# Kernel tuning notes

Hardware: AMD Instinct MI355X
Metric: run time of the kernel (lower is better)

## Reference

```python
import jax, jax.numpy as jnp
import numpy as np

HID = 128      # hidden_dim
CDIM = 128     # c_dim
NBLK = 5       # n_blocks
RESO = 32      # grid_resolution
G = RESO ** 3  # number of voxels
B, T = 2, 100000


def setup_inputs() -> dict:
    key = jax.random.key(0)
    ks = jax.random.split(key, 8)
    return {
        "points": jax.random.normal(ks[0], (B, T, 3), jnp.float32),
        "index": jax.random.randint(ks[1], (B, 1, T), 0, G, dtype=jnp.int64),
        # fc_pos: Linear(3, 2*HID)
        "fc_pos_w": jax.random.normal(ks[2], (3, 2 * HID), jnp.float32) * 0.1,
        "fc_pos_b": jnp.zeros((2 * HID,), jnp.float32),
        # ResnetBlockFC(2*HID, HID) x NBLK: fc_0 (2H->H), fc_1 (H->H), shortcut (2H->H, no bias)
        "fc0_w": jax.random.normal(ks[3], (NBLK, 2 * HID, HID), jnp.float32) * 0.05,
        "fc0_b": jnp.zeros((NBLK, HID), jnp.float32),
        "fc1_w": jax.random.normal(ks[4], (NBLK, HID, HID), jnp.float32) * 0.05,
        "fc1_b": jnp.zeros((NBLK, HID), jnp.float32),
        "sc_w": jax.random.normal(ks[5], (NBLK, 2 * HID, HID), jnp.float32) * 0.05,
        # fc_c: Linear(HID, CDIM)
        "fc_c_w": jax.random.normal(ks[6], (HID, CDIM), jnp.float32) * 0.05,
        "fc_c_b": jnp.zeros((CDIM,), jnp.float32),
    }


def _resnet_block(x, w0, b0, w1, b1, ws):
    # ResnetBlockFC: net = fc_0(relu(x)); dx = fc_1(relu(net)); out = shortcut(x) + dx
    net = jnp.maximum(x, 0.0) @ w0 + b0
    dx = jnp.maximum(net, 0.0) @ w1 + b1
    return x @ ws + dx


def reference(points, index, fc_pos_w, fc_pos_b, fc0_w, fc0_b, fc1_w, fc1_b, sc_w, fc_c_w, fc_c_b):
    idx = index[:, 0, :]  # [B, T]

    def pool_local(net):
        # scatter_max over voxels, then gather back per point
        seg = jax.vmap(lambda c_b, i_b: jax.ops.segment_max(c_b, i_b, num_segments=G))(net, idx)  # [B,G,H]
        return jnp.take_along_axis(seg, idx[:, :, None], axis=1)  # [B,T,H]; every gathered voxel is non-empty

    net = points @ fc_pos_w + fc_pos_b          # [B,T,2H]
    net = _resnet_block(net, fc0_w[0], fc0_b[0], fc1_w[0], fc1_b[0], sc_w[0])  # [B,T,H]
    for i in range(1, NBLK):
        pooled = pool_local(net)
        net = jnp.concatenate([net, pooled], axis=2)  # [B,T,2H]
        net = _resnet_block(net, fc0_w[i], fc0_b[i], fc1_w[i], fc1_b[i], sc_w[i])

    c = net @ fc_c_w + fc_c_b  # [B,T,CDIM]

    # generate_grid_features: scatter_mean into the 32^3 grid (zeros for empty voxels)
    sums = jax.vmap(lambda c_b, i_b: jax.ops.segment_sum(c_b, i_b, num_segments=G))(c, idx)  # [B,G,CDIM]
    cnts = jax.vmap(lambda i_b: jax.ops.segment_sum(jnp.ones((T,), c.dtype), i_b, num_segments=G))(idx)  # [B,G]
    cnts = cnts[:, :, None]
    mean = jnp.where(cnts > 0, sums / jnp.maximum(cnts, 1.0), 0.0)
    fea_grid = jnp.transpose(mean, (0, 2, 1)).reshape(B, CDIM, RESO, RESO, RESO)
    return fea_grid
```

## Files before the change

kernel.cpp:

```cpp
#include <hip/hip_runtime.h>

#define T_PTS 100000
#define NB 2
#define GCELLS 32768
#define NCELL (NB * GCELLS)
#define HID 128
#define MBLK 64
#define RBPB 1563
#define GRID_RB (NB * RBPB)

typedef __attribute__((ext_vector_type(8))) short bf16x8;
typedef __attribute__((ext_vector_type(4))) float f32x4;

#define MFMA16 __builtin_amdgcn_mfma_f32_16x16x32_bf16

__device__ __forceinline__ unsigned short bf16rne(float f) {
  unsigned u = __float_as_uint(f);
  return (unsigned short)((u + 0x7FFFu + ((u >> 16) & 1u)) >> 16);
}
__device__ __forceinline__ void bf16split(float f, unsigned short& h,
                                          unsigned short& l) {
  h = bf16rne(f);
  l = bf16rne(f - __uint_as_float(((unsigned)h) << 16));
}
__device__ __forceinline__ unsigned packhl(float f) {
  unsigned short h, l;
  bf16split(f, h, l);
  return (((unsigned)h) << 16) | (unsigned)l;
}

union U8 { bf16x8 v; unsigned u[4]; };

__device__ __forceinline__ void up2(unsigned w0, unsigned w1, unsigned& h,
                                    unsigned& l) {
  h = __builtin_amdgcn_perm(w1, w0, 0x07060302u);
  l = __builtin_amdgcn_perm(w1, w0, 0x05040100u);
}

__device__ __forceinline__ void relu2(unsigned qh, unsigned ql, unsigned& rh,
                                      unsigned& rl) {
  const unsigned keep = ((~qh >> 15) & 0x00010001u) * 0xFFFFu;
  rh = qh & keep;
  rl = ql & keep;
}

__device__ __forceinline__ void dma16(const unsigned* g, unsigned* l) {
  __builtin_amdgcn_global_load_lds(
      (const __attribute__((address_space(1))) unsigned*)g,
      (__attribute__((address_space(3))) unsigned*)l, 16, 0, 0);
}

template <int MODE>
__global__ __launch_bounds__(256, 4) void resblock_mfma(
    const void* __restrict__ srcv, const float* __restrict__ posw,
    const float* __restrict__ posb, const unsigned* __restrict__ cell,
    const int* __restrict__ idx, const unsigned short* __restrict__ w0p,
    const float* __restrict__ b0, const unsigned short* __restrict__ w1p,
    const float* __restrict__ b1, const unsigned short* __restrict__ swp,
    unsigned* __restrict__ net_out) {
  __shared__ unsigned lds32[8192];
  const int tid = threadIdx.x;
  const int lane = tid & 63;
  const int wid = tid >> 6;
  const int wc = wid;
  const int b = blockIdx.x / RBPB;
  const int t0 = (blockIdx.x % RBPB) * MBLK;
  const int valid = (T_PTS - t0 < MBLK) ? (T_PTS - t0) : MBLK;

  const int srow = wid * 16 + (lane & 15);
  const int skc4 = (lane >> 4) * 4;
  const int ptc = (t0 + srow < T_PTS) ? srow : (T_PTS - 1 - t0);
  const unsigned* nrowL = nullptr;
  const unsigned* crowL = nullptr;
  float pp0 = 0.f, pp1 = 0.f, pp2 = 0.f;
  if (MODE == 1) {
    const long prow = (long)b * T_PTS + t0 + ptc;
    nrowL = (const unsigned*)srcv + prow * HID;
    crowL = cell + ((long)b * GCELLS + idx[prow]) * HID;
  } else {
    const float* ppp = (const float*)srcv + ((long)b * T_PTS + t0 + ptc) * 3;
    pp0 = ppp[0]; pp1 = ppp[1]; pp2 = ppp[2];
  }

  auto stage_dma = [&](int ks) {
    unsigned* base = &lds32[((ks & 1) << 12) + wid * 256];
    const unsigned* rowp = (ks < 4) ? nrowL : crowL;
    const int ko = ((ks & 3) << 4) + skc4;
    dma16(rowp + ko, base);
    dma16(rowp + 64 + ko, base + 1024);
  };
  auto derive = [&](int ks) {
    const int db = ((ks & 1) << 12) + wid * 256 + lane * 4;
    uint4 qh = *(const uint4*)&lds32[db];
    uint4 ql = *(const uint4*)&lds32[db + 1024];
    uint4 rh, rl;
    relu2(qh.x, ql.x, rh.x, rl.x);
    relu2(qh.y, ql.y, rh.y, rl.y);
    relu2(qh.z, ql.z, rh.z, rl.z);
    relu2(qh.w, ql.w, rh.w, rl.w);
    *(uint4*)&lds32[db + 2048] = rh;
    *(uint4*)&lds32[db + 3072] = rl;
  };
  auto stage0 = [&](int ks) {
    const int kb = ks * 32 + (lane >> 4) * 8;
    float xv[8];
#pragma unroll
    for (int i = 0; i < 8; i += 4) {
      float4 wa = *(const float4*)(posw + kb + i);
      float4 wb = *(const float4*)(posw + 256 + kb + i);
      float4 wcc = *(const float4*)(posw + 512 + kb + i);
      float4 bb = *(const float4*)(posb + kb + i);
      xv[i + 0] = fmaf(pp0, wa.x, fmaf(pp1, wb.x, fmaf(pp2, wcc.x, bb.x)));
      xv[i + 1] = fmaf(pp0, wa.y, fmaf(pp1, wb.y, fmaf(pp2, wcc.y, bb.y)));
      xv[i + 2] = fmaf(pp0, wa.z, fmaf(pp1, wb.z, fmaf(pp2, wcc.z, bb.z)));
      xv[i + 3] = fmaf(pp0, wa.w, fmaf(pp1, wb.w, fmaf(pp2, wcc.w, bb.w)));
    }
    unsigned ph[8];
#pragma unroll
    for (int i = 0; i < 8; ++i) ph[i] = packhl(xv[i]);
    uint4 xh4, xl4, rh4, rl4;
    up2(ph[0], ph[1], xh4.x, xl4.x);
    up2(ph[2], ph[3], xh4.y, xl4.y);
    up2(ph[4], ph[5], xh4.z, xl4.z);
    up2(ph[6], ph[7], xh4.w, xl4.w);
    relu2(xh4.x, xl4.x, rh4.x, rl4.x);
    relu2(xh4.y, xl4.y, rh4.y, rl4.y);
    relu2(xh4.z, xl4.z, rh4.z, rl4.z);
    relu2(xh4.w, xl4.w, rh4.w, rl4.w);
    const int db = ((ks & 1) << 12) + wid * 256 + lane * 4;
    *(uint4*)&lds32[db] = xh4;
    *(uint4*)&lds32[db + 1024] = xl4;
    *(uint4*)&lds32[db + 2048] = rh4;
    *(uint4*)&lds32[db + 3072] = rl4;
  };
  auto load_B = [&](const unsigned short* base, int loOff, int ks, bf16x8* h,
                    bf16x8* l) {
#pragma unroll
    for (int nt = 0; nt < 2; ++nt) {
      const int fi = (ks * 8 + wc * 2 + nt) * 512 + lane * 8;
      h[nt] = *(const bf16x8*)(base + fi);
      l[nt] = *(const bf16x8*)(base + loOff + fi);
    }
  };

  f32x4 accy[4][2], acco[4][2];
#pragma unroll
  for (int i = 0; i < 4; ++i)
#pragma unroll
    for (int j = 0; j < 2; ++j) {
      f32x4 z = {0.f, 0.f, 0.f, 0.f};
      accy[i][j] = z;
      acco[i][j] = z;
    }

  if (MODE == 1) {
    stage_dma(0);
    asm volatile("s_waitcnt vmcnt(0)" ::: "memory");
    derive(0);
  } else {
    stage0(0);
  }
  __syncthreads();

#pragma unroll 1
  for (int ks = 0; ks < 8; ++ks) {
    const int sb = (ks & 1) << 12;
    bf16x8 bh[2], bl[2];
    load_B(w0p, 32768, ks, bh, bl);
    __builtin_amdgcn_s_setprio(1);
#pragma unroll
    for (int mt = 0; mt < 4; ++mt) {
      const unsigned* pr = &lds32[sb + 2048 + mt * 256 + lane * 4];
      bf16x8 rh = *(const bf16x8*)pr;
      bf16x8 rl = *(const bf16x8*)(pr + 1024);
#pragma unroll
      for (int nt = 0; nt < 2; ++nt) {
        accy[mt][nt] = MFMA16(rh, bh[nt], accy[mt][nt], 0, 0, 0);
        accy[mt][nt] = MFMA16(rh, bl[nt], accy[mt][nt], 0, 0, 0);
        accy[mt][nt] = MFMA16(rl, bh[nt], accy[mt][nt], 0, 0, 0);
      }
    }
    __builtin_amdgcn_s_setprio(0);
    load_B(swp, 32768, ks, bh, bl);
    if (MODE == 1 && ks < 7) stage_dma(ks + 1);
    __builtin_amdgcn_s_setprio(1);
#pragma unroll
    for (int mt = 0; mt < 4; ++mt) {
      const unsigned* px = &lds32[sb + mt * 256 + lane * 4];
      bf16x8 xh = *(const bf16x8*)px;
      bf16x8 xl = *(const bf16x8*)(px + 1024);
#pragma unroll
      for (int nt = 0; nt < 2; ++nt) {
        acco[mt][nt] = MFMA16(xh, bh[nt], acco[mt][nt], 0, 0, 0);
        acco[mt][nt] = MFMA16(xh, bl[nt], acco[mt][nt], 0, 0, 0);
        acco[mt][nt] = MFMA16(xl, bh[nt], acco[mt][nt], 0, 0, 0);
      }
    }
    __builtin_amdgcn_s_setprio(0);
    if (ks < 7) {
      if (MODE == 1) {
        asm volatile("s_waitcnt vmcnt(0)" ::: "memory");
        derive(ks + 1);
      } else {
        stage0(ks + 1);
      }
    }
    __syncthreads();
  }

  {
    float b0v[2];
#pragma unroll
    for (int nt = 0; nt < 2; ++nt)
      b0v[nt] = b0[wc * 32 + nt * 16 + (lane & 15)];
#pragma unroll
    for (int mt = 0; mt < 4; ++mt) {
#pragma unroll
      for (int nt = 0; nt < 2; ++nt) {
        const int c = wc * 32 + nt * 16 + (lane & 15);
        const int k2 = c >> 5;
        const int j = c & 7;
        const int lahi = ((c & 31) >> 3) * 16;
#pragma unroll
        for (int r = 0; r < 4; ++r) {
          float h = fmaxf(accy[mt][nt][r] + b0v[nt], 0.f);
          int la = lahi + (lane >> 4) * 4 + r;
          la ^= (la >> 3) & 7;
          lds32[((k2 * 4 + mt) * 64 + la) * 8 + j] = packhl(h);
        }
      }
    }
  }
  __syncthreads();

  {
    const int lar2 = lane ^ ((lane >> 3) & 7);
#pragma unroll
    for (int k2 = 0; k2 < 4; ++k2) {
      bf16x8 ch[2], cl[2];
      load_B(w1p, 16384, k2, ch, cl);
      __builtin_amdgcn_s_setprio(1);
#pragma unroll
      for (int mt = 0; mt < 4; ++mt) {
        const unsigned* p = &lds32[((k2 * 4 + mt) * 64 + lar2) * 8];
        uint4 q1 = *(const uint4*)p;
        uint4 q2 = *(const uint4*)(p + 4);
        unsigned q[8] = {q1.x, q1.y, q1.z, q1.w, q2.x, q2.y, q2.z, q2.w};
        U8 ah, al;
#pragma unroll
        for (int p2 = 0; p2 < 4; ++p2)
          up2(q[2 * p2], q[2 * p2 + 1], ah.u[p2], al.u[p2]);
#pragma unroll
        for (int nt = 0; nt < 2; ++nt) {
          acco[mt][nt] = MFMA16(ah.v, ch[nt], acco[mt][nt], 0, 0, 0);
          acco[mt][nt] = MFMA16(ah.v, cl[nt], acco[mt][nt], 0, 0, 0);
          acco[mt][nt] = MFMA16(al.v, ch[nt], acco[mt][nt], 0, 0, 0);
        }
      }
      __builtin_amdgcn_s_setprio(0);
    }
  }

  {
    float b1v[2];
#pragma unroll
    for (int nt = 0; nt < 2; ++nt)
      b1v[nt] = b1[wc * 32 + nt * 16 + (lane & 15)];
#pragma unroll
    for (int mt = 0; mt < 4; ++mt) {
#pragma unroll
      for (int r = 0; r < 4; ++r) {
        const int row = mt * 16 + (lane >> 4) * 4 + r;
        if (row < valid) {
          unsigned short* op =
              (unsigned short*)(net_out + ((long)b * T_PTS + t0 + row) * HID);
          unsigned short h, l;
          bf16split(acco[mt][0][r] + b1v[0], h, l);
          op[wc * 32 + (lane & 15)] = h;
          op[128 + wc * 32 + (lane & 15)] = l;
          bf16split(acco[mt][1][r] + b1v[1], h, l);
          op[wc * 32 + 16 + (lane & 15)] = h;
          op[128 + wc * 32 + 16 + (lane & 15)] = l;
        }
      }
    }
  }
}

__global__ __launch_bounds__(256, 4) void final_mfma(
    unsigned* __restrict__ net, const unsigned short* __restrict__ wcp,
    const float* __restrict__ bc) {
  __shared__ unsigned lds32[4096];
  const int tid = threadIdx.x;
  const int lane = tid & 63;
  const int wid = tid >> 6;
  const int wc = wid;
  const int b = blockIdx.x / RBPB;
  const int t0 = (blockIdx.x % RBPB) * MBLK;
  const int valid = (T_PTS - t0 < MBLK) ? (T_PTS - t0) : MBLK;

  const int srow = wid * 16 + (lane & 15);
  const int skc4 = (lane >> 4) * 4;
  const int ptc = (t0 + srow < T_PTS) ? srow : (T_PTS - 1 - t0);
  const unsigned* nrowL = net + ((long)b * T_PTS + t0 + ptc) * HID;

  auto stage = [&](int ks) {
    unsigned* base = &lds32[((ks & 1) << 11) + wid * 256];
    const int ko = (ks << 4) + skc4;
    dma16(nrowL + ko, base);
    dma16(nrowL + 64 + ko, base + 1024);
  };
  auto load_B = [&](int ks, bf16x8* h, bf16x8* l) {
#pragma unroll
    for (int nt = 0; nt < 2; ++nt) {
      const int fi = (ks * 8 + wc * 2 + nt) * 512 + lane * 8;
      h[nt] = *(const bf16x8*)(wcp + fi);
      l[nt] = *(const bf16x8*)(wcp + 16384 + fi);
    }
  };

  f32x4 acc[4][2];
#pragma unroll
  for (int i = 0; i < 4; ++i)
#pragma unroll
    for (int j = 0; j < 2; ++j) {
      f32x4 z = {0.f, 0.f, 0.f, 0.f};
      acc[i][j] = z;
    }

  stage(0);
  __syncthreads();

#pragma unroll 1
  for (int ks = 0; ks < 4; ++ks) {
    const int sb = (ks & 1) << 11;
    bf16x8 ch[2], cl[2];
    load_B(ks, ch, cl);
    if (ks < 3) stage(ks + 1);
    __builtin_amdgcn_s_setprio(1);
#pragma unroll
    for (int mt = 0; mt < 4; ++mt) {
      const unsigned* px = &lds32[sb + mt * 256 + lane * 4];
      bf16x8 xh = *(const bf16x8*)px;
      bf16x8 xl = *(const bf16x8*)(px + 1024);
#pragma unroll
      for (int nt = 0; nt < 2; ++nt) {
        acc[mt][nt] = MFMA16(xh, ch[nt], acc[mt][nt], 0, 0, 0);
        acc[mt][nt] = MFMA16(xh, cl[nt], acc[mt][nt], 0, 0, 0);
        acc[mt][nt] = MFMA16(xl, ch[nt], acc[mt][nt], 0, 0, 0);
      }
    }
    __builtin_amdgcn_s_setprio(0);
    __syncthreads();
  }

  float* fout = (float*)net;
  float bcv[2];
#pragma unroll
  for (int nt = 0; nt < 2; ++nt)
    bcv[nt] = bc[wc * 32 + nt * 16 + (lane & 15)];
#pragma unroll
  for (int mt = 0; mt < 4; ++mt) {
#pragma unroll
    for (int r = 0; r < 4; ++r) {
      const int row = mt * 16 + (lane >> 4) * 4 + r;
      if (row < valid) {
        float* op = fout + ((long)b * T_PTS + t0 + row) * HID;
        op[wc * 32 + (lane & 15)] = acc[mt][0][r] + bcv[0];
        op[wc * 32 + 16 + (lane & 15)] = acc[mt][1][r] + bcv[1];
      }
    }
  }
}

__global__ void pack_weights(const float* __restrict__ fc0,
                             const float* __restrict__ fc1,
                             const float* __restrict__ sc,
                             const float* __restrict__ fcc,
                             unsigned short* __restrict__ w0p,
                             unsigned short* __restrict__ w1p,
                             unsigned short* __restrict__ swp,
                             unsigned short* __restrict__ wcp) {
  int gid = blockIdx.x * 256 + threadIdx.x;
  const float* src;
  unsigned short* dst;
  int K, e;
  if (gid < 163840) { src = fc0; dst = w0p; K = 256; e = gid; }
  else if (gid < 327680) { src = sc; dst = swp; K = 256; e = gid - 163840; }
  else if (gid < 409600) { src = fc1; dst = w1p; K = 128; e = gid - 327680; }
  else if (gid < 425984) { src = fcc; dst = wcp; K = 128; e = gid - 409600; }
  else return;
  const int mat = e / (K * 128);
  const int r = e - mat * K * 128;
  const int k = r >> 7, n = r & 127;
  const float x = src[e];
  unsigned short hi, lo;
  bf16split(x, hi, lo);
  const int ks = k >> 5, lg = (k >> 3) & 3, j = k & 7;
  const int l = lg * 16 + (n & 15), nt = n >> 4;
  unsigned short* mb = dst + (long)mat * K * 256;
  const int off = ((ks * 8 + nt) * 64 + l) * 8 + j;
  mb[off] = hi;
  mb[off + K * 128] = lo;
}

__global__ void zero_i32(int* __restrict__ p, int n) {
  const int i = blockIdx.x * 256 + threadIdx.x;
  if (i < n) p[i] = 0;
}

__global__ void count_csr(const int* __restrict__ idx, int* __restrict__ curs) {
  const int gid = blockIdx.x * 256 + threadIdx.x;
  if (gid >= NB * T_PTS) return;
  const int b = gid / T_PTS;
  atomicAdd(&curs[b * GCELLS + idx[gid]], 1);
}

__global__ __launch_bounds__(1024) void scan_csr(const int* __restrict__ cnt,
                                                 int* __restrict__ offsets) {
  __shared__ int part[1024];
  const int t = threadIdx.x;
  const int base = t * (NCELL / 1024);
  int s = 0;
  for (int i = 0; i < NCELL / 1024; ++i) s += cnt[base + i];
  part[t] = s;
  __syncthreads();
  for (int d = 1; d < 1024; d <<= 1) {
    int v = (t >= d) ? part[t - d] : 0;
    __syncthreads();
    part[t] += v;
    __syncthreads();
  }
  int run = (t == 0) ? 0 : part[t - 1];
  for (int i = 0; i < NCELL / 1024; ++i) {
    offsets[base + i] = run;
    run += cnt[base + i];
  }
  if (t == 1023) offsets[NCELL] = run;
}

__global__ void scatter_csr(const int* __restrict__ idx,
                            const int* __restrict__ offsets,
                            int* __restrict__ curs, int* __restrict__ perm) {
  const int gid = blockIdx.x * 256 + threadIdx.x;
  if (gid >= NB * T_PTS) return;
  const int b = gid / T_PTS;
  const int cellk = b * GCELLS + idx[gid];
  const int slot = offsets[cellk] + atomicAdd(&curs[cellk], 1);
  perm[slot] = gid;
}

__global__ __launch_bounds__(256) void pool_csr(const unsigned* __restrict__ net,
                                                const int* __restrict__ perm,
                                                const int* __restrict__ offsets,
                                                unsigned* __restrict__ cellf) {
  const int cellk = blockIdx.x * 4 + (threadIdx.x >> 6);
  const int lane = threadIdx.x & 63;
  const int s0 = offsets[cellk], s1 = offsets[cellk + 1];
  if (s0 >= s1) return;
  float m0 = -3.402823466e38f, m1 = -3.402823466e38f;
  unsigned h0 = 0u, l0 = 0u, h1 = 0u, l1 = 0u;
  for (int j = s0; j < s1; ++j) {
    const long row = perm[j];
    const unsigned* rp = net + row * HID;
    unsigned hi = rp[lane];
    unsigned lo = rp[64 + lane];
    float v0 = __uint_as_float(hi << 16) + __uint_as_float(lo << 16);
    float v1 = __uint_as_float(hi & 0xFFFF0000u) +
               __uint_as_float(lo & 0xFFFF0000u);
    if (v0 > m0) { m0 = v0; h0 = hi; l0 = lo; }
    if (v1 > m1) { m1 = v1; h1 = hi; l1 = lo; }
  }
  unsigned* cp = cellf + (long)cellk * HID;
  cp[lane] = (h0 & 0xFFFFu) | (h1 & 0xFFFF0000u);
  cp[64 + lane] = (l0 & 0xFFFFu) | (l1 & 0xFFFF0000u);
}

__global__ __launch_bounds__(256) void cellsum_csr(
    const float* __restrict__ c, const int* __restrict__ perm,
    const int* __restrict__ offsets, float* __restrict__ sums) {
  const int cellk = blockIdx.x * 4 + (threadIdx.x >> 6);
  const int lane = threadIdx.x & 63;
  const int s0 = offsets[cellk], s1 = offsets[cellk + 1];
  if (s0 >= s1) return;
  float2 m = {0.f, 0.f};
  for (int j = s0; j < s1; ++j) {
    const long row = perm[j];
    float2 v = *(const float2*)(c + row * HID + lane * 2);
    m.x += v.x;
    m.y += v.y;
  }
  *(float2*)(sums + (long)cellk * HID + lane * 2) = m;
}

__global__ void mean_kernel(const float* __restrict__ sums,
                            const int* __restrict__ offsets,
                            float* __restrict__ out) {
  const long gid = (long)blockIdx.x * 256 + threadIdx.x;
  if (gid >= (long)NB * HID * GCELLS) return;
  const int g = (int)(gid % GCELLS);
  const int c = (int)((gid / GCELLS) % HID);
  const int b = (int)(gid / ((long)HID * GCELLS));
  const int cellk = b * GCELLS + g;
  const int cnt = offsets[cellk + 1] - offsets[cellk];
  out[gid] = cnt > 0 ? sums[(long)cellk * HID + c] / (float)cnt : 0.f;
}

extern "C" void kernel_launch(void* const* d_in, const int* in_sizes, int n_in,
                              void* d_out, int out_size, void* d_ws,
                              size_t ws_size, hipStream_t stream) {
  const float* points = (const float*)d_in[0];
  const int* idx = (const int*)d_in[1];
  const float* fc_pos_w = (const float*)d_in[2];
  const float* fc_pos_b = (const float*)d_in[3];
  const float* fc0_w = (const float*)d_in[4];
  const float* fc0_b = (const float*)d_in[5];
  const float* fc1_w = (const float*)d_in[6];
  const float* fc1_b = (const float*)d_in[7];
  const float* sc_w = (const float*)d_in[8];
  const float* fc_c_w = (const float*)d_in[9];
  const float* fc_c_b = (const float*)d_in[10];
  float* out = (float*)d_out;

  const long NET_BYTES = (long)NB * T_PTS * HID * 4;
  const long CELL_BYTES = (long)NB * GCELLS * HID * 4;
  unsigned* net = (unsigned*)d_ws;
  unsigned* cellf = (unsigned*)((char*)d_ws + NET_BYTES);
  float* sums = (float*)cellf;
  int* offsets = (int*)((char*)d_ws + NET_BYTES + CELL_BYTES);

  unsigned short* packs = (unsigned short*)d_out;
  unsigned short* w0p = packs;
  unsigned short* swp = packs + 327680;
  unsigned short* w1p = packs + 655360;
  unsigned short* wcp = packs + 819200;
  int* curs = (int*)((char*)d_out + (2l << 20));
  int* perm = (int*)((char*)d_out + (3l << 20));

  const int GRID_PTS = (NB * T_PTS + 255) / 256;
  const int GRID_ZERO = (NCELL + 255) / 256;
  const int GRID_CELL = NCELL / 4;
  const int GRID_MEAN = NB * HID * GCELLS / 256;

  pack_weights<<<1664, 256, 0, stream>>>(fc0_w, fc1_w, sc_w, fc_c_w, w0p, w1p,
                                         swp, wcp);

  zero_i32<<<GRID_ZERO, 256, 0, stream>>>(curs, NCELL);
  count_csr<<<GRID_PTS, 256, 0, stream>>>(idx, curs);
  scan_csr<<<1, 1024, 0, stream>>>(curs, offsets);
  zero_i32<<<GRID_ZERO, 256, 0, stream>>>(curs, NCELL);
  scatter_csr<<<GRID_PTS, 256, 0, stream>>>(idx, offsets, curs, perm);

  resblock_mfma<0><<<GRID_RB, 256, 0, stream>>>(
      points, fc_pos_w, fc_pos_b, nullptr, nullptr, w0p, fc0_b, w1p, fc1_b,
      swp, net);

  for (int i = 1; i < 5; ++i) {
    pool_csr<<<GRID_CELL, 256, 0, stream>>>(net, perm, offsets, cellf);
    resblock_mfma<1><<<GRID_RB, 256, 0, stream>>>(
        net, nullptr, nullptr, cellf, idx, w0p + (long)i * 65536,
        fc0_b + i * HID, w1p + (long)i * 32768, fc1_b + i * HID,
        swp + (long)i * 65536, net);
  }

  final_mfma<<<GRID_RB, 256, 0, stream>>>(net, wcp, fc_c_b);
  cellsum_csr<<<GRID_CELL, 256, 0, stream>>>((const float*)net, perm, offsets,
                                             sums);
  mean_kernel<<<GRID_MEAN, 256, 0, stream>>>(sums, offsets, out);
}
```

Baseline: 794.5 us.

## Apply ReLU in registers and merge fc_0 and shortcut MFMA loops

Drops the separate LDS pass that wrote ReLU'd hi/lo bf16 copies of each activation tile. The ReLU is now applied in registers right after the shared LDS read, and the fc_0 and shortcut MFMA chains run in a single loop. Both weight fragment sets are loaded up front, and the LDS double buffer shrinks by half. This removes LDS traffic and a wait-and-derive step per k-slice, but adds register pressure. It also drops the explicit vmcnt wait after the global-to-LDS DMA, so correctness depends on the barrier covering that transfer.

After: 799.6 us. Within noise of the previous version (+0.6%).

```diff
diff --git a/kernel.cpp b/kernel.cpp
--- a/kernel.cpp
+++ b/kernel.cpp
@@ -83,23 +83,11 @@
   }
 
   auto stage_dma = [&](int ks) {
-    unsigned* base = &lds32[((ks & 1) << 12) + wid * 256];
+    unsigned* base = &lds32[((ks & 1) << 11) + wid * 256];
     const unsigned* rowp = (ks < 4) ? nrowL : crowL;
     const int ko = ((ks & 3) << 4) + skc4;
     dma16(rowp + ko, base);
     dma16(rowp + 64 + ko, base + 1024);
-  };
-  auto derive = [&](int ks) {
-    const int db = ((ks & 1) << 12) + wid * 256 + lane * 4;
-    uint4 qh = *(const uint4*)&lds32[db];
-    uint4 ql = *(const uint4*)&lds32[db + 1024];
-    uint4 rh, rl;
-    relu2(qh.x, ql.x, rh.x, rl.x);
-    relu2(qh.y, ql.y, rh.y, rl.y);
-    relu2(qh.z, ql.z, rh.z, rl.z);
-    relu2(qh.w, ql.w, rh.w, rl.w);
-    *(uint4*)&lds32[db + 2048] = rh;
-    *(uint4*)&lds32[db + 3072] = rl;
   };
   auto stage0 = [&](int ks) {
     const int kb = ks * 32 + (lane >> 4) * 8;
@@ -118,20 +106,14 @@
     unsigned ph[8];
 #pragma unroll
     for (int i = 0; i < 8; ++i) ph[i] = packhl(xv[i]);
-    uint4 xh4, xl4, rh4, rl4;
+    uint4 xh4, xl4;
     up2(ph[0], ph[1], xh4.x, xl4.x);
     up2(ph[2], ph[3], xh4.y, xl4.y);
     up2(ph[4], ph[5], xh4.z, xl4.z);
     up2(ph[6], ph[7], xh4.w, xl4.w);
-    relu2(xh4.x, xl4.x, rh4.x, rl4.x);
-    relu2(xh4.y, xl4.y, rh4.y, rl4.y);
-    relu2(xh4.z, xl4.z, rh4.z, rl4.z);
-    relu2(xh4.w, xl4.w, rh4.w, rl4.w);
-    const int db = ((ks & 1) << 12) + wid * 256 + lane * 4;
+    const int db = ((ks & 1) << 11) + wid * 256 + lane * 4;
     *(uint4*)&lds32[db] = xh4;
     *(uint4*)&lds32[db + 1024] = xl4;
-    *(uint4*)&lds32[db + 2048] = rh4;
-    *(uint4*)&lds32[db + 3072] = rl4;
   };
   auto load_B = [&](const unsigned short* base, int loOff, int ks, bf16x8* h,
                     bf16x8* l) {
@@ -155,8 +137,6 @@
 
   if (MODE == 1) {
     stage_dma(0);
-    asm volatile("s_waitcnt vmcnt(0)" ::: "memory");
-    derive(0);
   } else {
     stage0(0);
   }
@@ -164,47 +144,35 @@
 
 #pragma unroll 1
   for (int ks = 0; ks < 8; ++ks) {
-    const int sb = (ks & 1) << 12;
-    bf16x8 bh[2], bl[2];
-    load_B(w0p, 32768, ks, bh, bl);
-    __builtin_amdgcn_s_setprio(1);
-#pragma unroll
-    for (int mt = 0; mt < 4; ++mt) {
-      const unsigned* pr = &lds32[sb + 2048 + mt * 256 + lane * 4];
-      bf16x8 rh = *(const bf16x8*)pr;
-      bf16x8 rl = *(const bf16x8*)(pr + 1024);
-#pragma unroll
-      for (int nt = 0; nt < 2; ++nt) {
-        accy[mt][nt] = MFMA16(rh, bh[nt], accy[mt][nt], 0, 0, 0);
-        accy[mt][nt] = MFMA16(rh, bl[nt], accy[mt][nt], 0, 0, 0);
-        accy[mt][nt] = MFMA16(rl, bh[nt], accy[mt][nt], 0, 0, 0);
-      }
-    }
-    __builtin_amdgcn_s_setprio(0);
-    load_B(swp, 32768, ks, bh, bl);
+    const int sb = (ks & 1) << 11;
+    bf16x8 b1h[2], b1l[2], b2h[2], b2l[2];
+    load_B(w0p, 32768, ks, b1h, b1l);
+    load_B(swp, 32768, ks, b2h, b2l);
     if (MODE == 1 && ks < 7) stage_dma(ks + 1);
     __builtin_amdgcn_s_setprio(1);
 #pragma unroll
     for (int mt = 0; mt < 4; ++mt) {
       const unsigned* px = &lds32[sb + mt * 256 + lane * 4];
-      bf16x8 xh = *(const bf16x8*)px;
-      bf16x8 xl = *(const bf16x8*)(px + 1024);
+      U8 xh, xl, rh, rl;
+      xh.v = *(const bf16x8*)px;
+      xl.v = *(const bf16x8*)(px + 1024);
+#pragma unroll
+      for (int i = 0; i < 4; ++i) relu2(xh.u[i], xl.u[i], rh.u[i], rl.u[i]);
 #pragma unroll
       for (int nt = 0; nt < 2; ++nt) {
-        acco[mt][nt] = MFMA16(xh, bh[nt], acco[mt][nt], 0, 0, 0);
-        acco[mt][nt] = MFMA16(xh, bl[nt], acco[mt][nt], 0, 0, 0);
-        acco[mt][nt] = MFMA16(xl, bh[nt], acco[mt][nt], 0, 0, 0);
+        accy[mt][nt] = MFMA16(rh.v, b1h[nt], accy[mt][nt], 0, 0, 0);
+        accy[mt][nt] = MFMA16(rh.v, b1l[nt], accy[mt][nt], 0, 0, 0);
+        accy[mt][nt] = MFMA16(rl.v, b1h[nt], accy[mt][nt], 0, 0, 0);
+      }
+#pragma unroll
+      for (int nt = 0; nt < 2; ++nt) {
+        acco[mt][nt] = MFMA16(xh.v, b2h[nt], acco[mt][nt], 0, 0, 0);
+        acco[mt][nt] = MFMA16(xh.v, b2l[nt], acco[mt][nt], 0, 0, 0);
+        acco[mt][nt] = MFMA16(xl.v, b2h[nt], acco[mt][nt], 0, 0, 0);
       }
     }
     __builtin_amdgcn_s_setprio(0);
-    if (ks < 7) {
-      if (MODE == 1) {
-        asm volatile("s_waitcnt vmcnt(0)" ::: "memory");
-        derive(ks + 1);
-      } else {
-        stage0(ks + 1);
-      }
-    }
+    if (MODE == 0 && ks < 7) stage0(ks + 1);
     __syncthreads();
   }
 
```
